# Kernel tuning notes

Hardware: AMD Instinct MI355X
Metric: run time of the kernel (lower is better)

## Reference

```python
import jax, jax.numpy as jnp
from jax import lax
import numpy as np

SCALE, IN_C, OUT_C, KER, R = 2, 64, 64, 3, 4

def _tconv(x, w, b, s, ker):
    # PyTorch ConvTranspose2d(w: [in,out,k,k], padding=ker//2, stride=s, output_padding=s-1)
    # as a fractionally-strided conv: flip kernel, swap in/out channel axes.
    wk = jnp.flip(jnp.transpose(w, (1, 0, 2, 3)), (2, 3))  # [out,in,k,k]
    p = ker // 2
    y = lax.conv_general_dilated(
        x, wk, window_strides=(1, 1),
        padding=[(p, p + s - 1), (p, p + s - 1)],
        lhs_dilation=(s, s),
        dimension_numbers=('NCHW', 'OIHW', 'NCHW'))
    return y + b[None, :, None, None]

def setup_inputs() -> dict:
    key = jax.random.key(0)
    ks = jax.random.split(key, 8)
    B, H, W = 4, 256, 256
    x = jax.random.normal(ks[0], (B, IN_C, H, W), jnp.float32)
    m = (jax.random.uniform(ks[1], (B, 1, H * SCALE, W * SCALE)) > 0.5).astype(jnp.float32)
    inv_mask = 1.0 - m
    # params (std per module init; exact std irrelevant for correctness)
    high_w = jax.random.normal(ks[2], (IN_C, OUT_C, KER, KER), jnp.float32) * 0.001
    high_b = jnp.zeros((OUT_C,), jnp.float32)
    low1_w = jax.random.normal(ks[3], (IN_C // R, IN_C, 1, 1), jnp.float32) * np.sqrt(2.0 / (IN_C // R))
    low1_b = jnp.zeros((IN_C // R,), jnp.float32)
    low2_w = jax.random.normal(ks[4], (IN_C // R, OUT_C, KER, KER), jnp.float32) * 0.001
    low2_b = jnp.zeros((OUT_C,), jnp.float32)
    return {"x": x, "mask": m, "inv_mask": inv_mask,
            "high_w": high_w, "high_b": high_b,
            "low1_w": low1_w, "low1_b": low1_b,
            "low2_w": low2_w, "low2_b": low2_b}

def reference(x, mask, inv_mask, high_w, high_b, low1_w, low1_b, low2_w, low2_b):
    # high branch: full transposed conv, masked per upsampled pixel
    high = _tconv(x, high_w, high_b, SCALE, KER) * mask  # [B,out,2H,2W]
    # low branch: 1x1 channel reduction then transposed conv, complementary mask
    low = jnp.einsum('bchw,oc->bohw', x, low1_w[:, :, 0, 0]) + low1_b[None, :, None, None]
    low = _tconv(low, low2_w, low2_b, SCALE, KER) * inv_mask
    return high + low
```

## Files before the change

kernel.cpp:

```cpp
#include <hip/hip_runtime.h>


typedef unsigned short u16;
typedef unsigned int   u32;
typedef __bf16 bf16x8 __attribute__((ext_vector_type(8)));
typedef u16    u16x8  __attribute__((ext_vector_type(8)));
typedef float  f32x4  __attribute__((ext_vector_type(4)));

#define DEV static __device__ __forceinline__

DEV u16   f2bf(float f){ u32 u = __builtin_bit_cast(u32, f); u += 0x7FFF + ((u >> 16) & 1); return (u16)(u >> 16); }
DEV bf16x8 asb(u16x8 v){ return __builtin_bit_cast(bf16x8, v); }
#define MF(acc, A, B) acc = __builtin_amdgcn_mfma_f32_16x16x32_bf16(asb(A), asb(B), acc, 0, 0, 0)

__global__ __launch_bounds__(256) void wprep(const float* __restrict__ hw, const float* __restrict__ lw,
                                             u16* __restrict__ whi, u16* __restrict__ wlo)
{
  int t = blockIdx.x * 256 + threadIdx.x;
  if (t < 36864) {
    int e = t & 7, lane = (t >> 3) & 63, tile = (t >> 9) & 3, Q = (t >> 11) & 1, tap = t >> 12;
    int q = lane >> 4, n = lane & 15;
    int c = 32 * Q + 8 * q + e, och = 16 * tile + n;
    whi[t] = f2bf(hw[(c * 64 + och) * 9 + tap]);
  } else if (t < 47104) {
    int t2 = t - 36864;
    int e = t2 & 7, lane = (t2 >> 3) & 63, tile = (t2 >> 9) & 3, f = t2 >> 11;
    int q = lane >> 4, n = lane & 15, och = 16 * tile + n;
    const int ta[10] = {4, -1, 3, 5, 1, 7, 0, 2, 6, 8};
    int tap = ta[f * 2 + (q >> 1)];
    u16 v = 0;
    if (tap >= 0) { int c = 8 * (q & 1) + e; v = f2bf(lw[(c * 64 + och) * 9 + tap]); }
    wlo[t2] = v;
  }
}

__global__ __launch_bounds__(256) void xr_kernel(const float* __restrict__ x, const float* __restrict__ w1,
                                                 const float* __restrict__ b1, u16* __restrict__ xr)
{
  __shared__ float sw[1024];
  __shared__ float sb[16];
  for (int u = threadIdx.x; u < 1024; u += 256) { int r = u & 15, c = u >> 4; sw[u] = w1[r * 64 + c]; }
  if (threadIdx.x < 16) sb[threadIdx.x] = b1[threadIdx.x];
  __syncthreads();
  int t = blockIdx.x * 256 + threadIdx.x;
  const float* xp = x + ((size_t)(t >> 16) << 22) + (t & 65535);
  float acc[16];
  #pragma unroll
  for (int r = 0; r < 16; ++r) acc[r] = sb[r];
  #pragma unroll 4
  for (int c = 0; c < 64; ++c) {
    float xv = xp[(size_t)c << 16];
    #pragma unroll
    for (int r = 0; r < 16; ++r) acc[r] = fmaf(xv, sw[c * 16 + r], acc[r]);
  }
  u32 pk[8];
  #pragma unroll
  for (int k = 0; k < 8; ++k) pk[k] = (u32)f2bf(acc[2 * k]) | ((u32)f2bf(acc[2 * k + 1]) << 16);
  uint4* dst = (uint4*)(xr + (size_t)t * 16);
  dst[0] = make_uint4(pk[0], pk[1], pk[2], pk[3]);
  dst[1] = make_uint4(pk[4], pk[5], pk[6], pk[7]);
}

__global__ __launch_bounds__(256) void tconv_main(
    const float* __restrict__ x, const u16* __restrict__ xr,
    const u16* __restrict__ whi, const u16* __restrict__ wlo,
    const float* __restrict__ mask, const float* __restrict__ hbp,
    const float* __restrict__ lbp, float* __restrict__ out)
{
  __shared__ __attribute__((aligned(16))) u16 xs [2][68][72];
  __shared__ __attribute__((aligned(16))) u16 xrs[2][68][24];

  const int tid  = threadIdx.x;
  const int lane = tid & 63, wid = tid >> 6;
  const int j0 = blockIdx.x * 64;
  const int i  = blockIdx.y;
  const int b  = blockIdx.z;
  const int q  = lane >> 4, n = lane & 15;

  u16x8 bh[9][2], bl[5];
  {
    const u16x8* wh8 = (const u16x8*)whi;
    #pragma unroll
    for (int tap = 0; tap < 9; ++tap)
      #pragma unroll
      for (int Q = 0; Q < 2; ++Q)
        bh[tap][Q] = wh8[((tap * 2 + Q) * 4 + wid) * 64 + lane];
    const u16x8* wl8 = (const u16x8*)wlo;
    #pragma unroll
    for (int f = 0; f < 5; ++f) bl[f] = wl8[(f * 4 + wid) * 64 + lane];
  }
  float hb4[4], lb4[4];
  #pragma unroll
  for (int r = 0; r < 4; ++r) {
    hb4[r] = hbp[16 * wid + 4 * q + r];
    lb4[r] = lbp[16 * wid + 4 * q + r];
  }

  for (int idx = tid; idx < 2 * 64 * 32; idx += 256) {
    int cp = idx & 31, c = (idx >> 5) & 63, row = idx >> 11;
    int gi = i + row, col = cp * 2;
    float2 v = make_float2(0.f, 0.f);
    if (gi < 256) v = *(const float2*)&x[((size_t)b << 22) + ((size_t)c << 16) + (gi << 8) + (j0 + col)];
    xs[row][col    ][c] = f2bf(v.x);
    xs[row][col + 1][c] = f2bf(v.y);
  }
  if (tid < 128) {
    int row = tid >> 6, c = tid & 63, gi = i + row, gj = j0 + 64;
    float v = 0.f;
    if (gi < 256 && gj < 256) v = x[((size_t)b << 22) + ((size_t)c << 16) + (gi << 8) + gj];
    xs[row][64][c] = f2bf(v);
  }
  for (int u = tid; u < 1040; u += 256) {
    int row = (u >= 520) ? 1 : 0;
    int uu  = u - row * 520;
    int col = uu >> 3, rcp = uu & 7;
    int gi = i + row, gj = j0 + col;
    u32 v = 0;
    if (gi < 256 && gj < 256) v = *(const u32*)(xr + ((size_t)((b * 256 + gi) * 256 + gj)) * 16 + rcp * 2);
    *(u32*)&xrs[row][col][rcp * 2] = v;
  }
  if (tid < 136) {
    int row = tid / 68, col = tid % 68;
    *(uint4*)&xrs[row][col][16] = make_uint4(0, 0, 0, 0);
  }
  __syncthreads();

  #pragma unroll
  for (int jt = 0; jt < 64; jt += 16) {
    const int colb = jt + n;
    u16x8 ah[2][2][2];
    #pragma unroll
    for (int r = 0; r < 2; ++r)
      #pragma unroll
      for (int d = 0; d < 2; ++d)
        #pragma unroll
        for (int Q = 0; Q < 2; ++Q)
          ah[r][d][Q] = *(const u16x8*)&xs[r][colb + d][32 * Q + 8 * q];
    const int dq = (q < 2) ? 1 : 0;
    u16x8 lf0 = *(const u16x8*)&xrs[0 ][colb     ][(q < 2) ? 8 * (q & 1) : 16];
    u16x8 lf1 = *(const u16x8*)&xrs[0 ][colb + dq][8 * (q & 1)];
    u16x8 lf2 = *(const u16x8*)&xrs[dq][colb     ][8 * (q & 1)];
    u16x8 lf3 = *(const u16x8*)&xrs[1 ][colb + dq][8 * (q & 1)];

    auto epi2 = [&](f32x4 hi0, f32x4 lo0, f32x4 hi1, f32x4 lo1, int py) {
      int y  = 2 * i + py;
      int xc = 2 * (j0 + jt + n);
      float2 mk = *(const float2*)&mask[((b * 512 + y) << 9) + xc];
      #pragma unroll
      for (int reg = 0; reg < 4; ++reg) {
        int oc = 16 * wid + 4 * q + reg;
        float h0 = hi0[reg] + hb4[reg], l0 = lo0[reg] + lb4[reg];
        float h1 = hi1[reg] + hb4[reg], l1 = lo1[reg] + lb4[reg];
        float2 o;
        o.x = l0 + mk.x * (h0 - l0);
        o.y = l1 + mk.y * (h1 - l1);
        *(float2*)&out[((size_t)(b * 64 + oc) << 18) + ((size_t)y << 9) + xc] = o;
      }
    };

    const f32x4 z4 = {0.f, 0.f, 0.f, 0.f};
    f32x4 h0, l0, h1, l1;
    h0 = z4; l0 = z4;
    MF(h0, bh[4][0], ah[0][0][0]); MF(h0, bh[4][1], ah[0][0][1]);
    MF(l0, bl[0], lf0);
    h1 = z4; l1 = z4;
    MF(h1, bh[3][0], ah[0][1][0]); MF(h1, bh[3][1], ah[0][1][1]);
    MF(h1, bh[5][0], ah[0][0][0]); MF(h1, bh[5][1], ah[0][0][1]);
    MF(l1, bl[1], lf1);
    epi2(h0, l0, h1, l1, 0);
    h0 = z4; l0 = z4;
    MF(h0, bh[1][0], ah[1][0][0]); MF(h0, bh[1][1], ah[1][0][1]);
    MF(h0, bh[7][0], ah[0][0][0]); MF(h0, bh[7][1], ah[0][0][1]);
    MF(l0, bl[2], lf2);
    h1 = z4; l1 = z4;
    MF(h1, bh[0][0], ah[1][1][0]); MF(h1, bh[0][1], ah[1][1][1]);
    MF(h1, bh[2][0], ah[1][0][0]); MF(h1, bh[2][1], ah[1][0][1]);
    MF(h1, bh[6][0], ah[0][1][0]); MF(h1, bh[6][1], ah[0][1][1]);
    MF(h1, bh[8][0], ah[0][0][0]); MF(h1, bh[8][1], ah[0][0][1]);
    MF(l1, bl[3], lf3); MF(l1, bl[4], lf1);
    epi2(h0, l0, h1, l1, 1);
  }
}

extern "C" void kernel_launch(void* const* d_in, const int* in_sizes, int n_in,
                              void* d_out, int out_size, void* d_ws, size_t ws_size,
                              hipStream_t stream)
{
  const float* x    = (const float*)d_in[0];
  const float* mask = (const float*)d_in[1];
  const float* hw   = (const float*)d_in[3];
  const float* hb   = (const float*)d_in[4];
  const float* l1w  = (const float*)d_in[5];
  const float* l1b  = (const float*)d_in[6];
  const float* l2w  = (const float*)d_in[7];
  const float* l2b  = (const float*)d_in[8];
  float* out = (float*)d_out;
  u16* ws  = (u16*)d_ws;
  u16* xr  = ws;
  u16* whi = ws + 4194304;
  u16* wlo = whi + 36864;

  wprep<<<184, 256, 0, stream>>>(hw, l2w, whi, wlo);
  xr_kernel<<<1024, 256, 0, stream>>>(x, l1w, l1b, xr);
  tconv_main<<<dim3(4, 256, 4), 256, 0, stream>>>(x, xr, whi, wlo, mask, hb, l2b, out);
}
```

Measured before the change: 425.0 us.

## Fuse 1x1 channel reduction into main tconv kernel via MFMA on shared tile

Removes the separate xr_kernel, which re-read all of x and wrote a bf16 reduced tensor to global memory. The main kernel now computes the 16-channel reduction itself with MFMA from the bf16 x tile already staged in shared memory, and writes it into xrs. It adds an extra sync and some redundant MFMA work per block, including the halo column, in exchange for removing a full pass over x and the xr round trip. wprep also packs the 1x1 weights into MFMA fragment layout.

```diff
diff --git a/kernel.cpp b/kernel.cpp
--- a/kernel.cpp
+++ b/kernel.cpp
@@ -14,7 +14,9 @@
 #define MF(acc, A, B) acc = __builtin_amdgcn_mfma_f32_16x16x32_bf16(asb(A), asb(B), acc, 0, 0, 0)
 
 __global__ __launch_bounds__(256) void wprep(const float* __restrict__ hw, const float* __restrict__ lw,
-                                             u16* __restrict__ whi, u16* __restrict__ wlo)
+                                             const float* __restrict__ l1w,
+                                             u16* __restrict__ whi, u16* __restrict__ wlo,
+                                             u16* __restrict__ w1f)
 {
   int t = blockIdx.x * 256 + threadIdx.x;
   if (t < 36864) {
@@ -31,41 +33,20 @@
     u16 v = 0;
     if (tap >= 0) { int c = 8 * (q & 1) + e; v = f2bf(lw[(c * 64 + och) * 9 + tap]); }
     wlo[t2] = v;
+  } else if (t < 48128) {
+    int t3 = t - 47104;
+    int e = t3 & 7, lane = (t3 >> 3) & 63, Q = t3 >> 9;
+    int q = lane >> 4, n = lane & 15;
+    w1f[t3] = f2bf(l1w[n * 64 + 32 * Q + 8 * q + e]);
   }
 }
 
-__global__ __launch_bounds__(256) void xr_kernel(const float* __restrict__ x, const float* __restrict__ w1,
-                                                 const float* __restrict__ b1, u16* __restrict__ xr)
-{
-  __shared__ float sw[1024];
-  __shared__ float sb[16];
-  for (int u = threadIdx.x; u < 1024; u += 256) { int r = u & 15, c = u >> 4; sw[u] = w1[r * 64 + c]; }
-  if (threadIdx.x < 16) sb[threadIdx.x] = b1[threadIdx.x];
-  __syncthreads();
-  int t = blockIdx.x * 256 + threadIdx.x;
-  const float* xp = x + ((size_t)(t >> 16) << 22) + (t & 65535);
-  float acc[16];
-  #pragma unroll
-  for (int r = 0; r < 16; ++r) acc[r] = sb[r];
-  #pragma unroll 4
-  for (int c = 0; c < 64; ++c) {
-    float xv = xp[(size_t)c << 16];
-    #pragma unroll
-    for (int r = 0; r < 16; ++r) acc[r] = fmaf(xv, sw[c * 16 + r], acc[r]);
-  }
-  u32 pk[8];
-  #pragma unroll
-  for (int k = 0; k < 8; ++k) pk[k] = (u32)f2bf(acc[2 * k]) | ((u32)f2bf(acc[2 * k + 1]) << 16);
-  uint4* dst = (uint4*)(xr + (size_t)t * 16);
-  dst[0] = make_uint4(pk[0], pk[1], pk[2], pk[3]);
-  dst[1] = make_uint4(pk[4], pk[5], pk[6], pk[7]);
-}
-
 __global__ __launch_bounds__(256) void tconv_main(
-    const float* __restrict__ x, const u16* __restrict__ xr,
-    const u16* __restrict__ whi, const u16* __restrict__ wlo,
+    const float* __restrict__ x,
+    const u16* __restrict__ whi, const u16* __restrict__ wlo, const u16* __restrict__ w1f,
     const float* __restrict__ mask, const float* __restrict__ hbp,
-    const float* __restrict__ lbp, float* __restrict__ out)
+    const float* __restrict__ lbp, const float* __restrict__ l1bp,
+    float* __restrict__ out)
 {
   __shared__ __attribute__((aligned(16))) u16 xs [2][68][72];
   __shared__ __attribute__((aligned(16))) u16 xrs[2][68][24];
@@ -76,25 +57,6 @@
   const int i  = blockIdx.y;
   const int b  = blockIdx.z;
   const int q  = lane >> 4, n = lane & 15;
-
-  u16x8 bh[9][2], bl[5];
-  {
-    const u16x8* wh8 = (const u16x8*)whi;
-    #pragma unroll
-    for (int tap = 0; tap < 9; ++tap)
-      #pragma unroll
-      for (int Q = 0; Q < 2; ++Q)
-        bh[tap][Q] = wh8[((tap * 2 + Q) * 4 + wid) * 64 + lane];
-    const u16x8* wl8 = (const u16x8*)wlo;
-    #pragma unroll
-    for (int f = 0; f < 5; ++f) bl[f] = wl8[(f * 4 + wid) * 64 + lane];
-  }
-  float hb4[4], lb4[4];
-  #pragma unroll
-  for (int r = 0; r < 4; ++r) {
-    hb4[r] = hbp[16 * wid + 4 * q + r];
-    lb4[r] = lbp[16 * wid + 4 * q + r];
-  }
 
   for (int idx = tid; idx < 2 * 64 * 32; idx += 256) {
     int cp = idx & 31, c = (idx >> 5) & 63, row = idx >> 11;
@@ -110,18 +72,59 @@
     if (gi < 256 && gj < 256) v = x[((size_t)b << 22) + ((size_t)c << 16) + (gi << 8) + gj];
     xs[row][64][c] = f2bf(v);
   }
-  for (int u = tid; u < 1040; u += 256) {
-    int row = (u >= 520) ? 1 : 0;
-    int uu  = u - row * 520;
-    int col = uu >> 3, rcp = uu & 7;
-    int gi = i + row, gj = j0 + col;
-    u32 v = 0;
-    if (gi < 256 && gj < 256) v = *(const u32*)(xr + ((size_t)((b * 256 + gi) * 256 + gj)) * 16 + rcp * 2);
-    *(u32*)&xrs[row][col][rcp * 2] = v;
-  }
   if (tid < 136) {
     int row = tid / 68, col = tid % 68;
     *(uint4*)&xrs[row][col][16] = make_uint4(0, 0, 0, 0);
+  }
+  __syncthreads();
+
+  {
+    const u16x8* w1f8 = (const u16x8*)w1f;
+    u16x8 aw0 = w1f8[lane], aw1 = w1f8[64 + lane];
+    float b14[4];
+    #pragma unroll
+    for (int r = 0; r < 4; ++r) b14[r] = l1bp[4 * q + r];
+    #pragma unroll
+    for (int tt = 0; tt < 3; ++tt) {
+      int tile = wid + 4 * tt;
+      if (tile < 9) {
+        int p = 16 * tile + n;
+        int row = (p >= 72) ? 1 : 0;
+        int col = p - 72 * row;
+        int colr = (col < 68) ? col : 67;
+        f32x4 d = {0.f, 0.f, 0.f, 0.f};
+        MF(d, aw0, *(const u16x8*)&xs[row][colr][8 * q]);
+        MF(d, aw1, *(const u16x8*)&xs[row][colr][32 + 8 * q]);
+        if (col < 65) {
+          int gi = i + row, gj = j0 + col;
+          u32 pk0 = 0, pk1 = 0;
+          if (gi < 256 && gj < 256) {
+            pk0 = (u32)f2bf(d[0] + b14[0]) | ((u32)f2bf(d[1] + b14[1]) << 16);
+            pk1 = (u32)f2bf(d[2] + b14[2]) | ((u32)f2bf(d[3] + b14[3]) << 16);
+          }
+          *(uint2*)&xrs[row][col][4 * q] = make_uint2(pk0, pk1);
+        }
+      }
+    }
+  }
+
+  u16x8 bh[9][2], bl[5];
+  {
+    const u16x8* wh8 = (const u16x8*)whi;
+    #pragma unroll
+    for (int tap = 0; tap < 9; ++tap)
+      #pragma unroll
+      for (int Q = 0; Q < 2; ++Q)
+        bh[tap][Q] = wh8[((tap * 2 + Q) * 4 + wid) * 64 + lane];
+    const u16x8* wl8 = (const u16x8*)wlo;
+    #pragma unroll
+    for (int f = 0; f < 5; ++f) bl[f] = wl8[(f * 4 + wid) * 64 + lane];
+  }
+  float hb4[4], lb4[4];
+  #pragma unroll
+  for (int r = 0; r < 4; ++r) {
+    hb4[r] = hbp[16 * wid + 4 * q + r];
+    lb4[r] = lbp[16 * wid + 4 * q + r];
   }
   __syncthreads();
 
@@ -196,11 +199,10 @@
   const float* l2b  = (const float*)d_in[8];
   float* out = (float*)d_out;
   u16* ws  = (u16*)d_ws;
-  u16* xr  = ws;
-  u16* whi = ws + 4194304;
+  u16* whi = ws;
   u16* wlo = whi + 36864;
-
-  wprep<<<184, 256, 0, stream>>>(hw, l2w, whi, wlo);
-  xr_kernel<<<1024, 256, 0, stream>>>(x, l1w, l1b, xr);
-  tconv_main<<<dim3(4, 256, 4), 256, 0, stream>>>(x, xr, whi, wlo, mask, hb, l2b, out);
+  u16* w1f = whi + 47104;
+
+  wprep<<<188, 256, 0, stream>>>(hw, l2w, l1w, whi, wlo, w1f);
+  tconv_main<<<dim3(4, 256, 4), 256, 0, stream>>>(x, whi, wlo, w1f, mask, hb, l2b, l1b, out);
 }
```

Result: faster. 411.2 us (-3.3%).
